# Performance work log

Hardware: AMD Instinct MI355X
Metric: run time of the kernel (lower is better)

Reference implementation:

```python
import jax, jax.numpy as jnp
import numpy as np

N_NODES = 50000
N_EDGES = 800000
IN_DIM = 64
EDGE_DIM = 32
OUT_DIM = 64


def setup_inputs() -> dict:
    key = jax.random.key(0)
    ks = jax.random.split(key, 7)
    x = jax.random.normal(ks[0], (N_NODES, IN_DIM), dtype=jnp.float32)
    edge_index = jax.random.randint(ks[1], (2, N_EDGES), 0, N_NODES, dtype=jnp.int64)
    edge_attr = jax.random.normal(ks[2], (N_EDGES, EDGE_DIM), dtype=jnp.float32)
    scale_msg = 1.0 / np.sqrt(IN_DIM + EDGE_DIM)
    scale_self = 1.0 / np.sqrt(IN_DIM)
    msg_w = jax.random.normal(ks[3], (IN_DIM + EDGE_DIM, OUT_DIM), dtype=jnp.float32) * scale_msg
    msg_b = jax.random.normal(ks[4], (OUT_DIM,), dtype=jnp.float32) * scale_msg
    self_w = jax.random.normal(ks[5], (IN_DIM, OUT_DIM), dtype=jnp.float32) * scale_self
    self_b = jax.random.normal(ks[6], (OUT_DIM,), dtype=jnp.float32) * scale_self
    return {"x": x, "edge_index": edge_index, "edge_attr": edge_attr,
            "msg_w": msg_w, "msg_b": msg_b, "self_w": self_w, "self_b": self_b}


def reference(x, edge_index, edge_attr, msg_w, msg_b, self_w, self_b):
    src = edge_index[0]
    dst = edge_index[1]
    n = x.shape[0]
    # gather source features, concat edge attrs, message linear: [E, out]
    msg_in = jnp.concatenate([x[src], edge_attr], axis=1)
    messages = msg_in @ msg_w + msg_b
    # scatter-mean over destination nodes
    agg = jax.ops.segment_sum(messages, dst, num_segments=n)
    deg = jax.ops.segment_sum(jnp.ones((dst.shape[0],), dtype=x.dtype), dst, num_segments=n)
    deg = jnp.maximum(deg, 1.0)[:, None]
    agg = agg / deg
    return x @ self_w + self_b + agg
```

## Files before the change

### kernel.cpp

```cpp
#include <hip/hip_runtime.h>


constexpr int N_NODES  = 50000;
constexpr int N_EDGES  = 800000;
constexpr int IN_DIM   = 64;
constexpr int EDGE_DIM = 32;
constexpr int OUT_DIM  = 64;
constexpr int CAP      = 48;
constexpr int OVF_CAP  = 65536;

using vf4 = __attribute__((ext_vector_type(4))) float;
using vi2 = __attribute__((ext_vector_type(2))) int;

__device__ __forceinline__ void place_one(int dst, int e, int src,
                                          int* cnt, int2* buckets,
                                          int4* ovf, int* ovf_cur) {
    const int pos = atomicAdd(&cnt[dst], 1);
    if (pos < CAP) {
        buckets[(size_t)dst * CAP + pos] = make_int2(e, src);
    } else {
        const int o = atomicAdd(ovf_cur, 1);
        if (o < OVF_CAP) ovf[o] = make_int4(dst, e, src, 0);
    }
}

__global__ __launch_bounds__(256) void place_bucket_k(
    const int* __restrict__ ei, int* cnt, int2* __restrict__ buckets,
    int4* __restrict__ ovf, int* ovf_cur)
{
    const int t = blockIdx.x * 256 + threadIdx.x;
    if (t * 4 + 3 < N_EDGES) {
        const int4 d4 = ((const int4*)(ei + N_EDGES))[t];
        const int4 s4 = ((const int4*)ei)[t];
        place_one(d4.x, 4 * t + 0, s4.x, cnt, buckets, ovf, ovf_cur);
        place_one(d4.y, 4 * t + 1, s4.y, cnt, buckets, ovf, ovf_cur);
        place_one(d4.z, 4 * t + 2, s4.z, cnt, buckets, ovf, ovf_cur);
        place_one(d4.w, 4 * t + 3, s4.w, cnt, buckets, ovf, ovf_cur);
    } else {
        for (int e = t * 4; e < min(t * 4 + 4, N_EDGES); ++e)
            place_one(ei[N_EDGES + e], e, ei[e], cnt, buckets, ovf, ovf_cur);
    }
}

__global__ __launch_bounds__(256) void aggregate_bucket_k(
    const float* __restrict__ x, const float* __restrict__ ea,
    const int2* __restrict__ buckets, const int* __restrict__ cnt,
    const int4* __restrict__ ovf, const int* __restrict__ ovf_cur,
    float* __restrict__ sum_x, float* __restrict__ sum_ea)
{
    const int lane   = threadIdx.x & 63;
    const int wave   = (blockIdx.x * blockDim.x + threadIdx.x) >> 6;
    const int nwaves = (gridDim.x * blockDim.x) >> 6;

    const int grpx = lane >> 4, colx = lane & 15;
    const int grpe = lane >> 3, cole = lane & 7;

    for (int n0 = wave * 2; n0 < N_NODES; n0 += nwaves * 2) {
        const int  nA   = __builtin_amdgcn_readfirstlane(n0);
        const bool hasB = (n0 + 1 < N_NODES);
        const int  nB   = nA + 1;

        const int cFA = __builtin_amdgcn_readfirstlane(cnt[nA]);
        const int cFB = hasB ? __builtin_amdgcn_readfirstlane(cnt[nB]) : 0;
        const int cA  = min(cFA, CAP);
        const int cB  = min(cFB, CAP);

        int eA = 0, srcA = 0, eB = 0, srcB = 0;
        if (lane < cA) {
            const vi2 p = __builtin_nontemporal_load(
                (const vi2*)buckets + (size_t)nA * CAP + lane);
            eA = p.x; srcA = p.y;
        }
        if (lane < cB) {
            const vi2 p = __builtin_nontemporal_load(
                (const vi2*)buckets + (size_t)nB * CAP + lane);
            eB = p.x; srcB = p.y;
        }

        vf4 axA = {0,0,0,0}, aeA = {0,0,0,0};
        vf4 axB = {0,0,0,0}, aeB = {0,0,0,0};

        const int mMax = max(cA, cB);
        for (int j = 0; j < mMax; j += 16) {
            const int jx0 = j +  0 + grpx, jx1 = j +  4 + grpx;
            const int jx2 = j +  8 + grpx, jx3 = j + 12 + grpx;
            const int je0 = j +  0 + grpe, je1 = j +  8 + grpe;
            const int sA0 = __shfl(srcA, jx0), sA1 = __shfl(srcA, jx1);
            const int sA2 = __shfl(srcA, jx2), sA3 = __shfl(srcA, jx3);
            const int sB0 = __shfl(srcB, jx0), sB1 = __shfl(srcB, jx1);
            const int sB2 = __shfl(srcB, jx2), sB3 = __shfl(srcB, jx3);
            const int fA0 = __shfl(eA, je0),   fA1 = __shfl(eA, je1);
            const int fB0 = __shfl(eB, je0),   fB1 = __shfl(eB, je1);

            vf4 xA0 = {0,0,0,0}, xA1 = {0,0,0,0}, xA2 = {0,0,0,0}, xA3 = {0,0,0,0};
            vf4 xB0 = {0,0,0,0}, xB1 = {0,0,0,0}, xB2 = {0,0,0,0}, xB3 = {0,0,0,0};
            vf4 eA0v = {0,0,0,0}, eA1v = {0,0,0,0};
            vf4 eB0v = {0,0,0,0}, eB1v = {0,0,0,0};

            if (jx0 < cA) xA0 = ((const vf4*)(x + (size_t)sA0 * IN_DIM))[colx];
            if (jx1 < cA) xA1 = ((const vf4*)(x + (size_t)sA1 * IN_DIM))[colx];
            if (jx2 < cA) xA2 = ((const vf4*)(x + (size_t)sA2 * IN_DIM))[colx];
            if (jx3 < cA) xA3 = ((const vf4*)(x + (size_t)sA3 * IN_DIM))[colx];
            if (jx0 < cB) xB0 = ((const vf4*)(x + (size_t)sB0 * IN_DIM))[colx];
            if (jx1 < cB) xB1 = ((const vf4*)(x + (size_t)sB1 * IN_DIM))[colx];
            if (jx2 < cB) xB2 = ((const vf4*)(x + (size_t)sB2 * IN_DIM))[colx];
            if (jx3 < cB) xB3 = ((const vf4*)(x + (size_t)sB3 * IN_DIM))[colx];
            if (je0 < cA) eA0v = __builtin_nontemporal_load(
                (const vf4*)(ea + (size_t)fA0 * EDGE_DIM) + cole);
            if (je1 < cA) eA1v = __builtin_nontemporal_load(
                (const vf4*)(ea + (size_t)fA1 * EDGE_DIM) + cole);
            if (je0 < cB) eB0v = __builtin_nontemporal_load(
                (const vf4*)(ea + (size_t)fB0 * EDGE_DIM) + cole);
            if (je1 < cB) eB1v = __builtin_nontemporal_load(
                (const vf4*)(ea + (size_t)fB1 * EDGE_DIM) + cole);

            axA += (xA0 + xA1) + (xA2 + xA3);
            axB += (xB0 + xB1) + (xB2 + xB3);
            aeA += eA0v + eA1v;
            aeB += eB0v + eB1v;
        }

        if (cFA > CAP || cFB > CAP) {
            const int novf = min(__builtin_amdgcn_readfirstlane(*ovf_cur), OVF_CAP);
            for (int i = 0; i < novf; ++i) {
                const int4 v = ovf[i];
                const bool mA = (v.x == nA), mB = hasB && (v.x == nB);
                if (mA || mB) {
                    if (grpx == 0) {
                        const vf4 t = ((const vf4*)(x + (size_t)v.z * IN_DIM))[colx];
                        if (mA) axA += t; else axB += t;
                    }
                    if (grpe == 0) {
                        const vf4 t = ((const vf4*)(ea + (size_t)v.y * EDGE_DIM))[cole];
                        if (mA) aeA += t; else aeB += t;
                    }
                }
            }
        }

#pragma unroll
        for (int mask = 16; mask < 64; mask <<= 1) {
            axA.x += __shfl_xor(axA.x, mask); axA.y += __shfl_xor(axA.y, mask);
            axA.z += __shfl_xor(axA.z, mask); axA.w += __shfl_xor(axA.w, mask);
            axB.x += __shfl_xor(axB.x, mask); axB.y += __shfl_xor(axB.y, mask);
            axB.z += __shfl_xor(axB.z, mask); axB.w += __shfl_xor(axB.w, mask);
        }
#pragma unroll
        for (int mask = 8; mask < 64; mask <<= 1) {
            aeA.x += __shfl_xor(aeA.x, mask); aeA.y += __shfl_xor(aeA.y, mask);
            aeA.z += __shfl_xor(aeA.z, mask); aeA.w += __shfl_xor(aeA.w, mask);
            aeB.x += __shfl_xor(aeB.x, mask); aeB.y += __shfl_xor(aeB.y, mask);
            aeB.z += __shfl_xor(aeB.z, mask); aeB.w += __shfl_xor(aeB.w, mask);
        }

        if (lane < 16) ((vf4*)(sum_x + (size_t)nA * IN_DIM))[lane] = axA;
        if (lane < 8)  ((vf4*)(sum_ea + (size_t)nA * EDGE_DIM))[lane] = aeA;
        if (hasB) {
            if (lane < 16) ((vf4*)(sum_x + (size_t)nB * IN_DIM))[lane] = axB;
            if (lane < 8)  ((vf4*)(sum_ea + (size_t)nB * EDGE_DIM))[lane] = aeB;
        }
    }
}

__global__ __launch_bounds__(64) void finalize64_k(
    const float* __restrict__ x, const float* sum_x_in,
    const float* __restrict__ sum_ea, const int* __restrict__ cnt,
    const float* __restrict__ msg_w, const float* __restrict__ msg_b,
    const float* __restrict__ self_w, const float* __restrict__ self_b,
    float* out)
{
    const int c = threadIdx.x;

    float wm[96];
    float wsf[64];
#pragma unroll
    for (int k = 0; k < 96; ++k) wm[k] = msg_w[k * OUT_DIM + c];
#pragma unroll
    for (int k = 0; k < 64; ++k) wsf[k] = self_w[k * OUT_DIM + c];
    const float mb = msg_b[c];
    const float sb = self_b[c];

    for (int n0 = blockIdx.x; n0 < N_NODES; n0 += gridDim.x) {
        const int n = __builtin_amdgcn_readfirstlane(n0);

        const float4* r1 = (const float4*)(sum_x_in + (size_t)n * IN_DIM);
        const float4* r2 = (const float4*)(sum_ea   + (size_t)n * EDGE_DIM);
        const float4* r3 = (const float4*)(x        + (size_t)n * IN_DIM);
        const int d = cnt[n];

        float am0 = 0.f, am1 = 0.f, am2 = 0.f, am3 = 0.f;
        float as0 = 0.f, as1 = 0.f, as2 = 0.f, as3 = 0.f;
#pragma unroll
        for (int q = 0; q < 16; ++q) {
            const float4 v = r1[q];
            am0 = fmaf(v.x, wm[4 * q + 0], am0);
            am1 = fmaf(v.y, wm[4 * q + 1], am1);
            am2 = fmaf(v.z, wm[4 * q + 2], am2);
            am3 = fmaf(v.w, wm[4 * q + 3], am3);
        }
#pragma unroll
        for (int q = 0; q < 8; ++q) {
            const float4 v = r2[q];
            am0 = fmaf(v.x, wm[64 + 4 * q + 0], am0);
            am1 = fmaf(v.y, wm[64 + 4 * q + 1], am1);
            am2 = fmaf(v.z, wm[64 + 4 * q + 2], am2);
            am3 = fmaf(v.w, wm[64 + 4 * q + 3], am3);
        }
#pragma unroll
        for (int q = 0; q < 16; ++q) {
            const float4 v = r3[q];
            as0 = fmaf(v.x, wsf[4 * q + 0], as0);
            as1 = fmaf(v.y, wsf[4 * q + 1], as1);
            as2 = fmaf(v.z, wsf[4 * q + 2], as2);
            as3 = fmaf(v.w, wsf[4 * q + 3], as3);
        }

        const float inv  = 1.0f / (float)max(d, 1);
        const float bsel = (d > 0) ? 1.0f : 0.0f;
        const float am   = (am0 + am1) + (am2 + am3);
        const float as   = (as0 + as1) + (as2 + as3);

        out[(size_t)n * OUT_DIM + c] = as + sb + am * inv + mb * bsel;
    }
}

__global__ __launch_bounds__(768) void scatter_fb_k(
    const float* __restrict__ x, const int* __restrict__ ei,
    const float* __restrict__ ea, float* sum_x, float* sum_ea, int* deg)
{
    const int t  = threadIdx.x;
    const int el = t / 96;
    const int k  = t - el * 96;
    const int e  = blockIdx.x * 8 + el;
    if (e >= N_EDGES) return;
    const int dst = ei[N_EDGES + e];
    if (k < IN_DIM) {
        const int src = ei[e];
        atomicAdd(&sum_x[dst * IN_DIM + k], x[src * IN_DIM + k]);
        if (k == 0) atomicAdd(&deg[dst], 1);
    } else {
        const int kk = k - IN_DIM;
        atomicAdd(&sum_ea[dst * EDGE_DIM + kk], ea[e * EDGE_DIM + kk]);
    }
}

extern "C" void kernel_launch(void* const* d_in, const int* in_sizes, int n_in,
                              void* d_out, int out_size, void* d_ws, size_t ws_size,
                              hipStream_t stream) {
    const float* x      = (const float*)d_in[0];
    const int*   ei     = (const int*)d_in[1];
    const float* ea     = (const float*)d_in[2];
    const float* msg_w  = (const float*)d_in[3];
    const float* msg_b  = (const float*)d_in[4];
    const float* self_w = (const float*)d_in[5];
    const float* self_b = (const float*)d_in[6];

    float* out = (float*)d_out;

    int*   cnt     = (int*)d_ws;
    int*   ovf_cur = cnt + N_NODES;
    int2*  buckets = (int2*)(cnt + N_NODES + 16);
    int4*  ovf     = (int4*)(buckets + (size_t)N_NODES * CAP);
    float* sum_ea  = (float*)(ovf + OVF_CAP);
    const size_t need_bucket =
        ((size_t)N_NODES + 16 + 2 * (size_t)N_NODES * CAP + 4 * (size_t)OVF_CAP +
         (size_t)N_NODES * EDGE_DIM) * sizeof(int);

    if (ws_size >= need_bucket) {
        hipMemsetAsync(cnt, 0, (N_NODES + 16) * sizeof(int), stream);
        place_bucket_k<<<(N_EDGES / 4 + 255) / 256, 256, 0, stream>>>(
            ei, cnt, buckets, ovf, ovf_cur);
        aggregate_bucket_k<<<(N_NODES / 2 + 3) / 4, 256, 0, stream>>>(
            x, ea, buckets, cnt, ovf, ovf_cur, out, sum_ea);
        finalize64_k<<<4096, 64, 0, stream>>>(
            x, out, sum_ea, cnt, msg_w, msg_b, self_w, self_b, out);
    } else {
        float* fb_sum_ea = (float*)d_ws;
        int*   deg       = (int*)(fb_sum_ea + (size_t)N_NODES * EDGE_DIM);
        hipMemsetAsync(d_out, 0, (size_t)N_NODES * OUT_DIM * sizeof(float), stream);
        hipMemsetAsync(d_ws, 0, (size_t)N_NODES * (EDGE_DIM + 1) * sizeof(float), stream);
        scatter_fb_k<<<(N_EDGES + 7) / 8, 768, 0, stream>>>(
            x, ei, ea, out, fb_sum_ea, deg);
        finalize64_k<<<4096, 64, 0, stream>>>(
            x, out, fb_sum_ea, deg, msg_w, msg_b, self_w, self_b, out);
    }
}
```

Measured before the change: 280.3 us.

## Fuse aggregation with message and self linear transforms via LDS-staged weights

Merges the aggregate and finalize kernels. Each 512-thread block stages msg_w and self_w (40 KB) plus biases in LDS, then each wave computes the per-node 160x64 matvec straight from shared scratch after reducing neighbor sums. This removes the global round trip for sum_x/sum_ea and one kernel launch. In exchange the grid becomes persistent (768 blocks), the LDS footprint limits occupancy, and the serial per-wave matvec adds latency to the gather loop.

```diff
diff --git a/kernel.cpp b/kernel.cpp
--- a/kernel.cpp
+++ b/kernel.cpp
@@ -42,18 +42,37 @@
     }
 }
 
-__global__ __launch_bounds__(256) void aggregate_bucket_k(
+__global__ __launch_bounds__(512) void agg_fused_k(
     const float* __restrict__ x, const float* __restrict__ ea,
     const int2* __restrict__ buckets, const int* __restrict__ cnt,
     const int4* __restrict__ ovf, const int* __restrict__ ovf_cur,
-    float* __restrict__ sum_x, float* __restrict__ sum_ea)
+    const float* __restrict__ msg_w, const float* __restrict__ msg_b,
+    const float* __restrict__ self_w, const float* __restrict__ self_b,
+    float* __restrict__ out)
 {
-    const int lane   = threadIdx.x & 63;
-    const int wave   = (blockIdx.x * blockDim.x + threadIdx.x) >> 6;
-    const int nwaves = (gridDim.x * blockDim.x) >> 6;
+    __shared__ float w_lds[160 * 64];
+    __shared__ float b_lds[128];
+    __shared__ float s_scr[8][2][160];
+
+    const int tid = threadIdx.x;
+    for (int i = tid; i < 96 * 64 / 4; i += 512)
+        ((vf4*)w_lds)[i] = ((const vf4*)msg_w)[i];
+    for (int i = tid; i < 64 * 64 / 4; i += 512)
+        ((vf4*)(w_lds + 96 * 64))[i] = ((const vf4*)self_w)[i];
+    if (tid < 64)       b_lds[tid] = msg_b[tid];
+    else if (tid < 128) b_lds[tid] = self_b[tid - 64];
+    __syncthreads();
+
+    const int lane   = tid & 63;
+    const int w      = tid >> 6;
+    const int wave   = blockIdx.x * 8 + w;
+    const int nwaves = gridDim.x * 8;
 
     const int grpx = lane >> 4, colx = lane & 15;
     const int grpe = lane >> 3, cole = lane & 7;
+
+    const float mb = b_lds[lane];
+    const float sb = b_lds[64 + lane];
 
     for (int n0 = wave * 2; n0 < N_NODES; n0 += nwaves * 2) {
         const int  nA   = __builtin_amdgcn_readfirstlane(n0);
@@ -153,11 +172,40 @@
             aeB.z += __shfl_xor(aeB.z, mask); aeB.w += __shfl_xor(aeB.w, mask);
         }
 
-        if (lane < 16) ((vf4*)(sum_x + (size_t)nA * IN_DIM))[lane] = axA;
-        if (lane < 8)  ((vf4*)(sum_ea + (size_t)nA * EDGE_DIM))[lane] = aeA;
+        if (lane < 16) {
+            *(vf4*)&s_scr[w][0][4 * lane] = axA;
+            const vf4 vs = ((const vf4*)(x + (size_t)nA * IN_DIM))[lane];
+            *(vf4*)&s_scr[w][0][96 + 4 * lane] = vs;
+        }
+        if (lane < 8) *(vf4*)&s_scr[w][0][64 + 4 * lane] = aeA;
         if (hasB) {
-            if (lane < 16) ((vf4*)(sum_x + (size_t)nB * IN_DIM))[lane] = axB;
-            if (lane < 8)  ((vf4*)(sum_ea + (size_t)nB * EDGE_DIM))[lane] = aeB;
+            if (lane < 16) {
+                *(vf4*)&s_scr[w][1][4 * lane] = axB;
+                const vf4 vs = ((const vf4*)(x + (size_t)nB * IN_DIM))[lane];
+                *(vf4*)&s_scr[w][1][96 + 4 * lane] = vs;
+            }
+            if (lane < 8) *(vf4*)&s_scr[w][1][64 + 4 * lane] = aeB;
+        }
+        float amA = 0.f, amB = 0.f, asA = 0.f, asB = 0.f;
+#pragma unroll 8
+        for (int k = 0; k < 96; ++k) {
+            const float wv = w_lds[k * 64 + lane];
+            amA = fmaf(s_scr[w][0][k], wv, amA);
+            amB = fmaf(s_scr[w][1][k], wv, amB);
+        }
+#pragma unroll 8
+        for (int k = 0; k < 64; ++k) {
+            const float wv = w_lds[(96 + k) * 64 + lane];
+            asA = fmaf(s_scr[w][0][96 + k], wv, asA);
+            asB = fmaf(s_scr[w][1][96 + k], wv, asB);
+        }
+        const float invA = 1.0f / (float)max(cFA, 1);
+        const float bselA = (cFA > 0) ? 1.0f : 0.0f;
+        out[(size_t)nA * OUT_DIM + lane] = asA + sb + amA * invA + mb * bselA;
+        if (hasB) {
+            const float invB = 1.0f / (float)max(cFB, 1);
+            const float bselB = (cFB > 0) ? 1.0f : 0.0f;
+            out[(size_t)nB * OUT_DIM + lane] = asB + sb + amB * invB + mb * bselB;
         }
     }
 }
@@ -261,19 +309,17 @@
     int*   ovf_cur = cnt + N_NODES;
     int2*  buckets = (int2*)(cnt + N_NODES + 16);
     int4*  ovf     = (int4*)(buckets + (size_t)N_NODES * CAP);
-    float* sum_ea  = (float*)(ovf + OVF_CAP);
     const size_t need_bucket =
-        ((size_t)N_NODES + 16 + 2 * (size_t)N_NODES * CAP + 4 * (size_t)OVF_CAP +
-         (size_t)N_NODES * EDGE_DIM) * sizeof(int);
+        ((size_t)N_NODES + 16 + 2 * (size_t)N_NODES * CAP +
+         4 * (size_t)OVF_CAP) * sizeof(int);
 
     if (ws_size >= need_bucket) {
         hipMemsetAsync(cnt, 0, (N_NODES + 16) * sizeof(int), stream);
         place_bucket_k<<<(N_EDGES / 4 + 255) / 256, 256, 0, stream>>>(
             ei, cnt, buckets, ovf, ovf_cur);
-        aggregate_bucket_k<<<(N_NODES / 2 + 3) / 4, 256, 0, stream>>>(
-            x, ea, buckets, cnt, ovf, ovf_cur, out, sum_ea);
-        finalize64_k<<<4096, 64, 0, stream>>>(
-            x, out, sum_ea, cnt, msg_w, msg_b, self_w, self_b, out);
+        agg_fused_k<<<768, 512, 0, stream>>>(
+            x, ea, buckets, cnt, ovf, ovf_cur,
+            msg_w, msg_b, self_w, self_b, out);
     } else {
         float* fb_sum_ea = (float*)d_ws;
         int*   deg       = (int*)(fb_sum_ea + (size_t)N_NODES * EDGE_DIM);
```

New measurement: 274.4 us. 2.1% less time.

## Load node rows cooperatively and broadcast via readlane, two nodes per wave

Applied to the files above, without the earlier changes.

The finalize kernel now loads each node's input rows with one vector load per lane across the wave and broadcasts elements with readlane. Previously every lane re-read the whole row from memory. Each wave handles two nodes per iteration, reusing the register-resident weights, and the launch uses 256-thread blocks with four waves each. Readlane produces scalar values, so this adds SALU/VALU transfer work. The two-node interleave also raises register pressure.

```diff
diff --git a/kernel.cpp b/kernel.cpp
--- a/kernel.cpp
+++ b/kernel.cpp
@@ -11,6 +11,10 @@
 
 using vf4 = __attribute__((ext_vector_type(4))) float;
 using vi2 = __attribute__((ext_vector_type(2))) int;
+
+__device__ __forceinline__ float rl(float v, int srclane) {
+    return __int_as_float(__builtin_amdgcn_readlane(__float_as_int(v), srclane));
+}
 
 __device__ __forceinline__ void place_one(int dst, int e, int src,
                                           int* cnt, int2* buckets,
@@ -162,65 +166,95 @@
     }
 }
 
-__global__ __launch_bounds__(64) void finalize64_k(
+__global__ __launch_bounds__(256, 2) void finalize_v3_k(
     const float* __restrict__ x, const float* sum_x_in,
     const float* __restrict__ sum_ea, const int* __restrict__ cnt,
     const float* __restrict__ msg_w, const float* __restrict__ msg_b,
     const float* __restrict__ self_w, const float* __restrict__ self_b,
     float* out)
 {
-    const int c = threadIdx.x;
+    const int lane = threadIdx.x & 63;
+    const int wid  = blockIdx.x * 4 + (threadIdx.x >> 6);
+    const int nw   = gridDim.x * 4;
 
     float wm[96];
     float wsf[64];
 #pragma unroll
-    for (int k = 0; k < 96; ++k) wm[k] = msg_w[k * OUT_DIM + c];
-#pragma unroll
-    for (int k = 0; k < 64; ++k) wsf[k] = self_w[k * OUT_DIM + c];
-    const float mb = msg_b[c];
-    const float sb = self_b[c];
-
-    for (int n0 = blockIdx.x; n0 < N_NODES; n0 += gridDim.x) {
-        const int n = __builtin_amdgcn_readfirstlane(n0);
-
-        const float4* r1 = (const float4*)(sum_x_in + (size_t)n * IN_DIM);
-        const float4* r2 = (const float4*)(sum_ea   + (size_t)n * EDGE_DIM);
-        const float4* r3 = (const float4*)(x        + (size_t)n * IN_DIM);
-        const int d = cnt[n];
-
-        float am0 = 0.f, am1 = 0.f, am2 = 0.f, am3 = 0.f;
-        float as0 = 0.f, as1 = 0.f, as2 = 0.f, as3 = 0.f;
+    for (int k = 0; k < 96; ++k) wm[k] = msg_w[k * OUT_DIM + lane];
+#pragma unroll
+    for (int k = 0; k < 64; ++k) wsf[k] = self_w[k * OUT_DIM + lane];
+    const float mb = msg_b[lane];
+    const float sb = self_b[lane];
+
+    for (int n0 = wid * 2; n0 < N_NODES; n0 += nw * 2) {
+        const int  nA   = __builtin_amdgcn_readfirstlane(n0);
+        const bool hasB = (n0 + 1 < N_NODES);
+        const int  nB   = nA + 1;
+
+        vf4 r1A = {0,0,0,0}, r2A = {0,0,0,0}, r3A = {0,0,0,0};
+        vf4 r1B = {0,0,0,0}, r2B = {0,0,0,0}, r3B = {0,0,0,0};
+        if (lane < 16) {
+            r1A = ((const vf4*)(sum_x_in + (size_t)nA * IN_DIM))[lane];
+            r3A = ((const vf4*)(x        + (size_t)nA * IN_DIM))[lane];
+        }
+        if (lane < 8) r2A = ((const vf4*)(sum_ea + (size_t)nA * EDGE_DIM))[lane];
+        if (hasB) {
+            if (lane < 16) {
+                r1B = ((const vf4*)(sum_x_in + (size_t)nB * IN_DIM))[lane];
+                r3B = ((const vf4*)(x        + (size_t)nB * IN_DIM))[lane];
+            }
+            if (lane < 8) r2B = ((const vf4*)(sum_ea + (size_t)nB * EDGE_DIM))[lane];
+        }
+        const int dA = cnt[nA];
+        const int dB = hasB ? cnt[nB] : 0;
+
+        float amA0 = 0.f, amA1 = 0.f, amB0 = 0.f, amB1 = 0.f;
+        float asA0 = 0.f, asA1 = 0.f, asB0 = 0.f, asB1 = 0.f;
+
 #pragma unroll
         for (int q = 0; q < 16; ++q) {
-            const float4 v = r1[q];
-            am0 = fmaf(v.x, wm[4 * q + 0], am0);
-            am1 = fmaf(v.y, wm[4 * q + 1], am1);
-            am2 = fmaf(v.z, wm[4 * q + 2], am2);
-            am3 = fmaf(v.w, wm[4 * q + 3], am3);
+            amA0 = fmaf(rl(r1A[0], q), wm[4 * q + 0], amA0);
+            amA1 = fmaf(rl(r1A[1], q), wm[4 * q + 1], amA1);
+            amA0 = fmaf(rl(r1A[2], q), wm[4 * q + 2], amA0);
+            amA1 = fmaf(rl(r1A[3], q), wm[4 * q + 3], amA1);
+            amB0 = fmaf(rl(r1B[0], q), wm[4 * q + 0], amB0);
+            amB1 = fmaf(rl(r1B[1], q), wm[4 * q + 1], amB1);
+            amB0 = fmaf(rl(r1B[2], q), wm[4 * q + 2], amB0);
+            amB1 = fmaf(rl(r1B[3], q), wm[4 * q + 3], amB1);
         }
 #pragma unroll
         for (int q = 0; q < 8; ++q) {
-            const float4 v = r2[q];
-            am0 = fmaf(v.x, wm[64 + 4 * q + 0], am0);
-            am1 = fmaf(v.y, wm[64 + 4 * q + 1], am1);
-            am2 = fmaf(v.z, wm[64 + 4 * q + 2], am2);
-            am3 = fmaf(v.w, wm[64 + 4 * q + 3], am3);
+            amA0 = fmaf(rl(r2A[0], q), wm[64 + 4 * q + 0], amA0);
+            amA1 = fmaf(rl(r2A[1], q), wm[64 + 4 * q + 1], amA1);
+            amA0 = fmaf(rl(r2A[2], q), wm[64 + 4 * q + 2], amA0);
+            amA1 = fmaf(rl(r2A[3], q), wm[64 + 4 * q + 3], amA1);
+            amB0 = fmaf(rl(r2B[0], q), wm[64 + 4 * q + 0], amB0);
+            amB1 = fmaf(rl(r2B[1], q), wm[64 + 4 * q + 1], amB1);
+            amB0 = fmaf(rl(r2B[2], q), wm[64 + 4 * q + 2], amB0);
+            amB1 = fmaf(rl(r2B[3], q), wm[64 + 4 * q + 3], amB1);
         }
 #pragma unroll
         for (int q = 0; q < 16; ++q) {
-            const float4 v = r3[q];
-            as0 = fmaf(v.x, wsf[4 * q + 0], as0);
-            as1 = fmaf(v.y, wsf[4 * q + 1], as1);
-            as2 = fmaf(v.z, wsf[4 * q + 2], as2);
-            as3 = fmaf(v.w, wsf[4 * q + 3], as3);
-        }
-
-        const float inv  = 1.0f / (float)max(d, 1);
-        const float bsel = (d > 0) ? 1.0f : 0.0f;
-        const float am   = (am0 + am1) + (am2 + am3);
-        const float as   = (as0 + as1) + (as2 + as3);
-
-        out[(size_t)n * OUT_DIM + c] = as + sb + am * inv + mb * bsel;
+            asA0 = fmaf(rl(r3A[0], q), wsf[4 * q + 0], asA0);
+            asA1 = fmaf(rl(r3A[1], q), wsf[4 * q + 1], asA1);
+            asA0 = fmaf(rl(r3A[2], q), wsf[4 * q + 2], asA0);
+            asA1 = fmaf(rl(r3A[3], q), wsf[4 * q + 3], asA1);
+            asB0 = fmaf(rl(r3B[0], q), wsf[4 * q + 0], asB0);
+            asB1 = fmaf(rl(r3B[1], q), wsf[4 * q + 1], asB1);
+            asB0 = fmaf(rl(r3B[2], q), wsf[4 * q + 2], asB0);
+            asB1 = fmaf(rl(r3B[3], q), wsf[4 * q + 3], asB1);
+        }
+
+        const float invA  = 1.0f / (float)max(dA, 1);
+        const float bselA = (dA > 0) ? 1.0f : 0.0f;
+        out[(size_t)nA * OUT_DIM + lane] =
+            (asA0 + asA1) + sb + (amA0 + amA1) * invA + mb * bselA;
+        if (hasB) {
+            const float invB  = 1.0f / (float)max(dB, 1);
+            const float bselB = (dB > 0) ? 1.0f : 0.0f;
+            out[(size_t)nB * OUT_DIM + lane] =
+                (asB0 + asB1) + sb + (amB0 + amB1) * invB + mb * bselB;
+        }
     }
 }
 
@@ -272,7 +306,7 @@
             ei, cnt, buckets, ovf, ovf_cur);
         aggregate_bucket_k<<<(N_NODES / 2 + 3) / 4, 256, 0, stream>>>(
             x, ea, buckets, cnt, ovf, ovf_cur, out, sum_ea);
-        finalize64_k<<<4096, 64, 0, stream>>>(
+        finalize_v3_k<<<512, 256, 0, stream>>>(
             x, out, sum_ea, cnt, msg_w, msg_b, self_w, self_b, out);
     } else {
         float* fb_sum_ea = (float*)d_ws;
@@ -281,7 +315,7 @@
         hipMemsetAsync(d_ws, 0, (size_t)N_NODES * (EDGE_DIM + 1) * sizeof(float), stream);
         scatter_fb_k<<<(N_EDGES + 7) / 8, 768, 0, stream>>>(
             x, ei, ea, out, fb_sum_ea, deg);
-        finalize64_k<<<4096, 64, 0, stream>>>(
+        finalize_v3_k<<<512, 256, 0, stream>>>(
             x, out, fb_sum_ea, deg, msg_w, msg_b, self_w, self_b, out);
     }
 }
```

Result: faster. 274.6 us (-2.0%).

## Restructure finalize to row-per-lane with uniform weight loads and separate sum_x buffer

Applied to the files above, without the earlier changes.

The finalize kernel switches from one node per 64-thread block, with weights held in per-thread registers, to one node per lane. Each wave covers 64 nodes and 32 output columns, and weight rows are read as wave-uniform scalar loads. Aggregated x sums now go to a dedicated workspace buffer instead of aliasing the output, which allows __restrict__ on all pointers. The aim is to cut per-node loop overhead, get coalesced vector stores, and raise occupancy. The cost is per-lane strided row reads of 384 bytes per node and 32 accumulators per thread.

```diff
diff --git a/kernel.cpp b/kernel.cpp
--- a/kernel.cpp
+++ b/kernel.cpp
@@ -162,65 +162,85 @@
     }
 }
 
-__global__ __launch_bounds__(64) void finalize64_k(
-    const float* __restrict__ x, const float* sum_x_in,
+__global__ __launch_bounds__(256) void finalize_v5_k(
+    const float* __restrict__ x, const float* __restrict__ sum_x_in,
     const float* __restrict__ sum_ea, const int* __restrict__ cnt,
     const float* __restrict__ msg_w, const float* __restrict__ msg_b,
     const float* __restrict__ self_w, const float* __restrict__ self_b,
-    float* out)
+    float* __restrict__ out)
 {
-    const int c = threadIdx.x;
-
-    float wm[96];
-    float wsf[64];
-#pragma unroll
-    for (int k = 0; k < 96; ++k) wm[k] = msg_w[k * OUT_DIM + c];
-#pragma unroll
-    for (int k = 0; k < 64; ++k) wsf[k] = self_w[k * OUT_DIM + c];
-    const float mb = msg_b[c];
-    const float sb = self_b[c];
-
-    for (int n0 = blockIdx.x; n0 < N_NODES; n0 += gridDim.x) {
-        const int n = __builtin_amdgcn_readfirstlane(n0);
-
-        const float4* r1 = (const float4*)(sum_x_in + (size_t)n * IN_DIM);
-        const float4* r2 = (const float4*)(sum_ea   + (size_t)n * EDGE_DIM);
-        const float4* r3 = (const float4*)(x        + (size_t)n * IN_DIM);
-        const int d = cnt[n];
-
-        float am0 = 0.f, am1 = 0.f, am2 = 0.f, am3 = 0.f;
-        float as0 = 0.f, as1 = 0.f, as2 = 0.f, as3 = 0.f;
-#pragma unroll
-        for (int q = 0; q < 16; ++q) {
-            const float4 v = r1[q];
-            am0 = fmaf(v.x, wm[4 * q + 0], am0);
-            am1 = fmaf(v.y, wm[4 * q + 1], am1);
-            am2 = fmaf(v.z, wm[4 * q + 2], am2);
-            am3 = fmaf(v.w, wm[4 * q + 3], am3);
-        }
-#pragma unroll
-        for (int q = 0; q < 8; ++q) {
-            const float4 v = r2[q];
-            am0 = fmaf(v.x, wm[64 + 4 * q + 0], am0);
-            am1 = fmaf(v.y, wm[64 + 4 * q + 1], am1);
-            am2 = fmaf(v.z, wm[64 + 4 * q + 2], am2);
-            am3 = fmaf(v.w, wm[64 + 4 * q + 3], am3);
-        }
-#pragma unroll
-        for (int q = 0; q < 16; ++q) {
-            const float4 v = r3[q];
-            as0 = fmaf(v.x, wsf[4 * q + 0], as0);
-            as1 = fmaf(v.y, wsf[4 * q + 1], as1);
-            as2 = fmaf(v.z, wsf[4 * q + 2], as2);
-            as3 = fmaf(v.w, wsf[4 * q + 3], as3);
-        }
-
-        const float inv  = 1.0f / (float)max(d, 1);
-        const float bsel = (d > 0) ? 1.0f : 0.0f;
-        const float am   = (am0 + am1) + (am2 + am3);
-        const float as   = (as0 + as1) + (as2 + as3);
-
-        out[(size_t)n * OUT_DIM + c] = as + sb + am * inv + mb * bsel;
+    const int lane   = threadIdx.x & 63;
+    const int wunit  = blockIdx.x * 4 + (threadIdx.x >> 6);
+    const int rowblk = wunit >> 1;
+    const int c0     = (wunit & 1) << 5;
+    const int n      = rowblk * 64 + lane;
+    const bool live  = (n < N_NODES);
+    const int  nn    = live ? n : 0;
+
+    const vf4* rx = (const vf4*)(sum_x_in + (size_t)nn * IN_DIM);
+    const vf4* re = (const vf4*)(sum_ea   + (size_t)nn * EDGE_DIM);
+    const vf4* rs = (const vf4*)(x        + (size_t)nn * IN_DIM);
+    const int  d  = cnt[nn];
+
+    float acc[32];
+#pragma unroll
+    for (int c = 0; c < 32; ++c) acc[c] = 0.f;
+
+#pragma unroll 2
+    for (int q = 0; q < 16; ++q) {
+        const vf4 v  = rx[q];
+        const int kb = __builtin_amdgcn_readfirstlane(4 * q);
+#pragma unroll
+        for (int i = 0; i < 4; ++i) {
+            const float  vi   = v[i];
+            const float* wrow = msg_w + (size_t)(kb + i) * OUT_DIM + c0;
+#pragma unroll
+            for (int c = 0; c < 32; ++c)
+                acc[c] = fmaf(vi, wrow[c], acc[c]);
+        }
+    }
+#pragma unroll 2
+    for (int q = 0; q < 8; ++q) {
+        const vf4 v  = re[q];
+        const int kb = __builtin_amdgcn_readfirstlane(64 + 4 * q);
+#pragma unroll
+        for (int i = 0; i < 4; ++i) {
+            const float  vi   = v[i];
+            const float* wrow = msg_w + (size_t)(kb + i) * OUT_DIM + c0;
+#pragma unroll
+            for (int c = 0; c < 32; ++c)
+                acc[c] = fmaf(vi, wrow[c], acc[c]);
+        }
+    }
+
+    const float inv  = 1.0f / (float)max(d, 1);
+    const float bsel = (d > 0) ? 1.0f : 0.0f;
+#pragma unroll
+    for (int c = 0; c < 32; ++c)
+        acc[c] = fmaf(acc[c], inv, msg_b[c0 + c] * bsel);
+
+#pragma unroll 2
+    for (int q = 0; q < 16; ++q) {
+        const vf4 v  = rs[q];
+        const int kb = __builtin_amdgcn_readfirstlane(4 * q);
+#pragma unroll
+        for (int i = 0; i < 4; ++i) {
+            const float  vi   = v[i];
+            const float* wrow = self_w + (size_t)(kb + i) * OUT_DIM + c0;
+#pragma unroll
+            for (int c = 0; c < 32; ++c)
+                acc[c] = fmaf(vi, wrow[c], acc[c]);
+        }
+    }
+#pragma unroll
+    for (int c = 0; c < 32; ++c) acc[c] += self_b[c0 + c];
+
+    if (live) {
+        float* op = out + (size_t)n * OUT_DIM + c0;
+#pragma unroll
+        for (int qq = 0; qq < 8; ++qq)
+            ((vf4*)op)[qq] = (vf4){acc[4 * qq + 0], acc[4 * qq + 1],
+                                   acc[4 * qq + 2], acc[4 * qq + 3]};
     }
 }
 
@@ -262,26 +282,31 @@
     int2*  buckets = (int2*)(cnt + N_NODES + 16);
     int4*  ovf     = (int4*)(buckets + (size_t)N_NODES * CAP);
     float* sum_ea  = (float*)(ovf + OVF_CAP);
+    float* sum_x   = sum_ea + (size_t)N_NODES * EDGE_DIM;
     const size_t need_bucket =
         ((size_t)N_NODES + 16 + 2 * (size_t)N_NODES * CAP + 4 * (size_t)OVF_CAP +
-         (size_t)N_NODES * EDGE_DIM) * sizeof(int);
+         (size_t)N_NODES * EDGE_DIM + (size_t)N_NODES * IN_DIM) * sizeof(int);
+
+    constexpr int FIN_BLOCKS = ((N_NODES + 63) / 64 * 2 + 3) / 4;
 
     if (ws_size >= need_bucket) {
         hipMemsetAsync(cnt, 0, (N_NODES + 16) * sizeof(int), stream);
         place_bucket_k<<<(N_EDGES / 4 + 255) / 256, 256, 0, stream>>>(
             ei, cnt, buckets, ovf, ovf_cur);
         aggregate_bucket_k<<<(N_NODES / 2 + 3) / 4, 256, 0, stream>>>(
-            x, ea, buckets, cnt, ovf, ovf_cur, out, sum_ea);
-        finalize64_k<<<4096, 64, 0, stream>>>(
-            x, out, sum_ea, cnt, msg_w, msg_b, self_w, self_b, out);
+            x, ea, buckets, cnt, ovf, ovf_cur, sum_x, sum_ea);
+        finalize_v5_k<<<FIN_BLOCKS, 256, 0, stream>>>(
+            x, sum_x, sum_ea, cnt, msg_w, msg_b, self_w, self_b, out);
     } else {
-        float* fb_sum_ea = (float*)d_ws;
+        float* fb_sum_x  = (float*)d_ws;
+        float* fb_sum_ea = fb_sum_x + (size_t)N_NODES * IN_DIM;
         int*   deg       = (int*)(fb_sum_ea + (size_t)N_NODES * EDGE_DIM);
-        hipMemsetAsync(d_out, 0, (size_t)N_NODES * OUT_DIM * sizeof(float), stream);
-        hipMemsetAsync(d_ws, 0, (size_t)N_NODES * (EDGE_DIM + 1) * sizeof(float), stream);
+        hipMemsetAsync(d_ws, 0,
+                       (size_t)N_NODES * (IN_DIM + EDGE_DIM + 1) * sizeof(float),
+                       stream);
         scatter_fb_k<<<(N_EDGES + 7) / 8, 768, 0, stream>>>(
-            x, ei, ea, out, fb_sum_ea, deg);
-        finalize64_k<<<4096, 64, 0, stream>>>(
-            x, out, fb_sum_ea, deg, msg_w, msg_b, self_w, self_b, out);
-    }
-}
+            x, ei, ea, fb_sum_x, fb_sum_ea, deg);
+        finalize_v5_k<<<FIN_BLOCKS, 256, 0, stream>>>(
+            x, fb_sum_x, fb_sum_ea, deg, msg_w, msg_b, self_w, self_b, out);
+    }
+}
```

After: 318.5 us. +13.6%, slower.
